# Kernel tuning notes

Measured on AMD Instinct MI355X. Metric: run time of the kernel, lower is better.

The kernel has to match this reference:

```python
import jax, jax.numpy as jnp
import numpy as np

E = 250000          # num_edges
T = 1500000         # num_triplets
H = 128             # hidden_dim
NB = 8              # num_bilinear
NS = 7              # num_spherical
NR = 6              # num_radial
OUT = 128           # output_dim


def silu(x):
    return x * jax.nn.sigmoid(x)


def setup_inputs() -> dict:
    key = jax.random.key(0)
    ks = jax.random.split(key, 24)
    s = 1.0 / np.sqrt(H)
    inp = {
        "x": jax.random.normal(ks[0], (E, H), jnp.float32),
        "rbf": jax.random.uniform(ks[1], (E, NR), jnp.float32),
        "sbf": jax.random.uniform(ks[2], (T, NS * NR), jnp.float32),
        "idx_kj": jax.random.randint(ks[3], (T,), 0, E, jnp.int32),
        "idx_ji": jax.random.randint(ks[4], (T,), 0, E, jnp.int32),
        # weights stored [in, out] (math identical to torch y = x @ W.T + b)
        "lin_rbf_w": jax.random.normal(ks[5], (NR, H), jnp.float32) * (1.0 / np.sqrt(NR)),
        "lin_sbf_w": jax.random.normal(ks[6], (NS * NR, NB), jnp.float32) * (1.0 / np.sqrt(NS * NR)),
        "lin_kj_w": jax.random.normal(ks[7], (H, H), jnp.float32) * s,
        "lin_kj_b": jnp.zeros((H,), jnp.float32),
        "lin_ji_w": jax.random.normal(ks[8], (H, H), jnp.float32) * s,
        "lin_ji_b": jnp.zeros((H,), jnp.float32),
        "W": jax.random.normal(ks[9], (H, NB, H), jnp.float32) * (2.0 / H),
        "rb_w1": jax.random.normal(ks[10], (H, H), jnp.float32) * s,
        "rb_b1": jnp.zeros((H,), jnp.float32),
        "rb_w2": jax.random.normal(ks[11], (H, H), jnp.float32) * s,
        "rb_b2": jnp.zeros((H,), jnp.float32),
        "lin_w": jax.random.normal(ks[12], (H, H), jnp.float32) * s,
        "lin_b": jnp.zeros((H,), jnp.float32),
        "ra1_w1": jax.random.normal(ks[13], (H, H), jnp.float32) * s,
        "ra1_b1": jnp.zeros((H,), jnp.float32),
        "ra1_w2": jax.random.normal(ks[14], (H, H), jnp.float32) * s,
        "ra1_b2": jnp.zeros((H,), jnp.float32),
        "ra2_w1": jax.random.normal(ks[15], (H, H), jnp.float32) * s,
        "ra2_b1": jnp.zeros((H,), jnp.float32),
        "ra2_w2": jax.random.normal(ks[16], (H, H), jnp.float32) * s,
        "ra2_b2": jnp.zeros((H,), jnp.float32),
        "lin_out_w": jax.random.normal(ks[17], (H, OUT), jnp.float32) * s,
        "lin_out_b": jnp.zeros((OUT,), jnp.float32),
    }
    return inp


def _residual(h, w1, b1, w2, b2):
    return h + silu(silu(h @ w1 + b1) @ w2 + b2)


def reference(x, rbf, sbf, idx_kj, idx_ji,
              lin_rbf_w, lin_sbf_w, lin_kj_w, lin_kj_b, lin_ji_w, lin_ji_b, W,
              rb_w1, rb_b1, rb_w2, rb_b2, lin_w, lin_b,
              ra1_w1, ra1_b1, ra1_w2, ra1_b2, ra2_w1, ra2_b1, ra2_w2, ra2_b2,
              lin_out_w, lin_out_b):
    rbf_h = rbf @ lin_rbf_w                      # [E, H]
    sbf_h = sbf @ lin_sbf_w                      # [T, NB]
    x_ji = silu(x @ lin_ji_w + lin_ji_b)         # [E, H]
    x_kj = silu(x @ lin_kj_w + lin_kj_b) * rbf_h # [E, H]
    xk = x_kj[idx_kj]                            # gather -> [T, H]
    # trilinear einsum 'wj,wl,ijl->wi' without materializing [T, NB, H]:
    # loop over the small bilinear axis (NB=8), each step a [T,H]@[H,H] matmul
    out_t = jnp.zeros_like(xk)
    for j in range(NB):
        out_t = out_t + sbf_h[:, j:j + 1] * (xk @ W[:, j, :].T)   # [T, H]
    agg = jax.ops.segment_sum(out_t, idx_ji, num_segments=x.shape[0])  # [E, H]
    h = x_ji + agg
    h = _residual(h, rb_w1, rb_b1, rb_w2, rb_b2)
    h = silu(h @ lin_w + lin_b) + x
    h = _residual(h, ra1_w1, ra1_b1, ra1_w2, ra1_b2)
    h = _residual(h, ra2_w1, ra2_b1, ra2_w2, ra2_b2)
    return silu(h @ lin_out_w + lin_out_b)
```

## Files before the change

kernel.cpp:

```cpp
#include <hip/hip_runtime.h>

#define EDGES 250000
#define TRIP  1500000
#define HD    128
#define NBIL  8
#define NSR   42
#define NRAD  6

__device__ __forceinline__ float silu_f(float v) {
  return v / (1.0f + __expf(-v));
}

#define GET4(v,i) ((i)==0?(v).x:((i)==1?(v).y:((i)==2?(v).z:(v).w)))


__global__ void k_hist(const int* __restrict__ idxji, int* __restrict__ hist) {
  const int t = blockIdx.x * 256 + threadIdx.x;
  if (t < TRIP) atomicAdd(&hist[idxji[t]], 1);
}

__global__ __launch_bounds__(256) void k_scan1(const int* __restrict__ hist, int* __restrict__ blks) {
  __shared__ int sd[256];
  const int tid = threadIdx.x;
  const long base = (long)blockIdx.x * 1024 + tid * 4;
  int s = 0;
#pragma unroll
  for (int u = 0; u < 4; ++u) { const long i = base + u; if (i < EDGES) s += hist[i]; }
  sd[tid] = s; __syncthreads();
  for (int off = 128; off > 0; off >>= 1) { if (tid < off) sd[tid] += sd[tid + off]; __syncthreads(); }
  if (tid == 0) blks[blockIdx.x] = sd[0];
}

__global__ __launch_bounds__(256) void k_scan2(int* __restrict__ blks, int n) {
  __shared__ int sd[256];
  const int tid = threadIdx.x;
  const int v = (tid < n) ? blks[tid] : 0;
  sd[tid] = v; __syncthreads();
  for (int off = 1; off < 256; off <<= 1) {
    const int t = (tid >= off) ? sd[tid - off] : 0;
    __syncthreads();
    sd[tid] += t;
    __syncthreads();
  }
  if (tid < n) blks[tid] = sd[tid] - v;
}

__global__ __launch_bounds__(256) void k_scan3(int* __restrict__ cursor, const int* __restrict__ blks,
                                               int* __restrict__ offs) {
  __shared__ int sd[256];
  const int tid = threadIdx.x;
  const long base = (long)blockIdx.x * 1024 + tid * 4;
  int v[4]; int s = 0;
#pragma unroll
  for (int u = 0; u < 4; ++u) { const long i = base + u; v[u] = (i < EDGES) ? cursor[i] : 0; s += v[u]; }
  sd[tid] = s; __syncthreads();
  for (int off = 1; off < 256; off <<= 1) {
    const int tv = (tid >= off) ? sd[tid - off] : 0;
    __syncthreads();
    sd[tid] += tv;
    __syncthreads();
  }
  int run = blks[blockIdx.x] + sd[tid] - s;
#pragma unroll
  for (int u = 0; u < 4; ++u) {
    const long i = base + u;
    if (i < EDGES) { offs[i] = run; cursor[i] = run; }
    run += v[u];
  }
  if (blockIdx.x == 0 && tid == 0) offs[EDGES] = TRIP;
}

__global__ void k_scatter(const int* __restrict__ idxji, const int* __restrict__ idxkj,
                          int* __restrict__ cursor, int* __restrict__ gkj, int* __restrict__ tpos) {
  const int t = blockIdx.x * 256 + threadIdx.x;
  if (t < TRIP) {
    const int e = idxji[t];
    const int pos = atomicAdd(&cursor[e], 1);
    gkj[pos] = idxkj[t];
    tpos[t] = pos;
  }
}


__global__ void k_wt(const float* __restrict__ W, float* __restrict__ wt) {
  const int idx = blockIdx.x * 256 + threadIdx.x;
  if (idx < NBIL * HD * HD) {
    const int i = idx & (HD - 1);
    const int k = idx >> 7;
    const int j = k >> 7;
    const int l = k & (HD - 1);
    wt[idx] = W[((long)i * NBIL + j) * HD + l];
  }
}


__global__ __launch_bounds__(256) void k_sbfh(const float* __restrict__ sbf,
    const float* __restrict__ sw, const int* __restrict__ tpos, float* __restrict__ outp) {
  __shared__ float ss[256 * NSR];
  __shared__ float wls[NSR * NBIL];
  const int tid = threadIdx.x;
  const long t0 = (long)blockIdx.x * 256;
  const long gbase = t0 * NSR;
  for (int idx = tid; idx < 256 * NSR; idx += 256) {
    const long gi = gbase + idx;
    ss[idx] = (gi < (long)TRIP * NSR) ? sbf[gi] : 0.f;
  }
  for (int idx = tid; idx < NSR * NBIL; idx += 256) wls[idx] = sw[idx];
  __syncthreads();
  const long t = t0 + tid;
  if (t < TRIP) {
    float o[NBIL] = {};
    for (int r = 0; r < NSR; ++r) {
      const float sv = ss[tid * NSR + r];
#pragma unroll
      for (int j = 0; j < NBIL; ++j) o[j] += sv * wls[r * NBIL + j];
    }
    const long p = tpos[t];
    *(float4*)(outp + p * 8) = make_float4(o[0], o[1], o[2], o[3]);
    *(float4*)(outp + p * 8 + 4) = make_float4(o[4], o[5], o[6], o[7]);
  }
}


__global__ __launch_bounds__(256, 4) void k_edge(const float* __restrict__ x,
    const float* __restrict__ rbf, const float* __restrict__ rbfw,
    const float* __restrict__ wji, const float* __restrict__ bji,
    const float* __restrict__ wkj, const float* __restrict__ bkj,
    float* __restrict__ xji, float* __restrict__ xkj) {
  __shared__ float xs[32][HD + 4];
  __shared__ float rbfs[32][NRAD];
  __shared__ float rws[NRAD][HD];
  const int tid = threadIdx.x;
  const long e0 = (long)blockIdx.x * 32;
  for (int idx = tid; idx < 32 * (HD / 4); idx += 256) {
    const int el = idx >> 5; const int k4 = (idx & 31) << 2;
    const long e = e0 + el;
    float4 v = make_float4(0.f, 0.f, 0.f, 0.f);
    if (e < EDGES) v = *(const float4*)(x + e * HD + k4);
    *(float4*)&xs[el][k4] = v;
  }
  for (int idx = tid; idx < 32 * NRAD; idx += 256) {
    const int el = idx / NRAD, r = idx % NRAD;
    const long e = e0 + el;
    rbfs[el][r] = (e < EDGES) ? rbf[e * NRAD + r] : 0.f;
  }
  for (int idx = tid; idx < NRAD * HD; idx += 256) rws[idx / HD][idx % HD] = rbfw[idx];
  __syncthreads();
  const int cg = tid & 15, eg = tid >> 4;
  const int i0 = cg * 8;
  float aj[2][8] = {}, ak[2][8] = {};
  for (int k = 0; k < HD; k += 4) {
    const float4 xv0 = *(const float4*)&xs[eg * 2 + 0][k];
    const float4 xv1 = *(const float4*)&xs[eg * 2 + 1][k];
#pragma unroll
    for (int dk = 0; dk < 4; ++dk) {
      const float4 j0 = *(const float4*)(wji + (long)(k + dk) * HD + i0);
      const float4 j1 = *(const float4*)(wji + (long)(k + dk) * HD + i0 + 4);
      const float4 q0 = *(const float4*)(wkj + (long)(k + dk) * HD + i0);
      const float4 q1 = *(const float4*)(wkj + (long)(k + dk) * HD + i0 + 4);
      const float a0 = GET4(xv0, dk), a1 = GET4(xv1, dk);
#pragma unroll
      for (int c = 0; c < 4; ++c) {
        const float wja = GET4(j0, c), wjb = GET4(j1, c);
        const float wka = GET4(q0, c), wkb = GET4(q1, c);
        aj[0][c] += a0 * wja; aj[0][c + 4] += a0 * wjb;
        aj[1][c] += a1 * wja; aj[1][c + 4] += a1 * wjb;
        ak[0][c] += a0 * wka; ak[0][c + 4] += a0 * wkb;
        ak[1][c] += a1 * wka; ak[1][c + 4] += a1 * wkb;
      }
    }
  }
  const float4 bj0 = *(const float4*)(bji + i0), bj1 = *(const float4*)(bji + i0 + 4);
  const float4 bk0 = *(const float4*)(bkj + i0), bk1 = *(const float4*)(bkj + i0 + 4);
#pragma unroll
  for (int a = 0; a < 2; ++a) {
    const int el = eg * 2 + a;
    const long e = e0 + el;
    if (e >= EDGES) continue;
    float rh[8];
#pragma unroll
    for (int c = 0; c < 8; ++c) rh[c] = 0.f;
#pragma unroll
    for (int r = 0; r < NRAD; ++r) {
      const float rv = rbfs[el][r];
#pragma unroll
      for (int c = 0; c < 8; ++c) rh[c] += rv * rws[r][i0 + c];
    }
    float oj[8], ok[8];
#pragma unroll
    for (int c = 0; c < 4; ++c) {
      oj[c]     = silu_f(aj[a][c]     + GET4(bj0, c));
      oj[c + 4] = silu_f(aj[a][c + 4] + GET4(bj1, c));
      ok[c]     = silu_f(ak[a][c]     + GET4(bk0, c)) * rh[c];
      ok[c + 4] = silu_f(ak[a][c + 4] + GET4(bk1, c)) * rh[c + 4];
    }
    *(float4*)(xji + e * HD + i0)     = make_float4(oj[0], oj[1], oj[2], oj[3]);
    *(float4*)(xji + e * HD + i0 + 4) = make_float4(oj[4], oj[5], oj[6], oj[7]);
    *(float4*)(xkj + e * HD + i0)     = make_float4(ok[0], ok[1], ok[2], ok[3]);
    *(float4*)(xkj + e * HD + i0 + 4) = make_float4(ok[4], ok[5], ok[6], ok[7]);
  }
}


#define FMA16(sA, sB, xv) do { \
  m[0]  += (sA).x * (xv).x;  m[1]  += (sA).x * (xv).y; \
  m[2]  += (sA).y * (xv).x;  m[3]  += (sA).y * (xv).y; \
  m[4]  += (sA).z * (xv).x;  m[5]  += (sA).z * (xv).y; \
  m[6]  += (sA).w * (xv).x;  m[7]  += (sA).w * (xv).y; \
  m[8]  += (sB).x * (xv).x;  m[9]  += (sB).x * (xv).y; \
  m[10] += (sB).y * (xv).x;  m[11] += (sB).y * (xv).y; \
  m[12] += (sB).z * (xv).x;  m[13] += (sB).z * (xv).y; \
  m[14] += (sB).w * (xv).x;  m[15] += (sB).w * (xv).y; } while (0)

#define ACCUM_SEGMENT(t0, t1) \
    int t = (t0); \
    for (; t + 4 <= (t1); t += 4) { \
      const int g0 = gkj[t], g1 = gkj[t + 1], g2 = gkj[t + 2], g3 = gkj[t + 3]; \
      const float2 x0 = *(const float2*)(xkj + (long)g0 * HD + l2); \
      const float2 x1 = *(const float2*)(xkj + (long)g1 * HD + l2); \
      const float2 x2 = *(const float2*)(xkj + (long)g2 * HD + l2); \
      const float2 x3 = *(const float2*)(xkj + (long)g3 * HD + l2); \
      const float4 sa0 = *(const float4*)(sbfp + (long)t * 8); \
      const float4 sb0 = *(const float4*)(sbfp + (long)t * 8 + 4); \
      const float4 sa1 = *(const float4*)(sbfp + (long)(t + 1) * 8); \
      const float4 sb1 = *(const float4*)(sbfp + (long)(t + 1) * 8 + 4); \
      const float4 sa2 = *(const float4*)(sbfp + (long)(t + 2) * 8); \
      const float4 sb2 = *(const float4*)(sbfp + (long)(t + 2) * 8 + 4); \
      const float4 sa3 = *(const float4*)(sbfp + (long)(t + 3) * 8); \
      const float4 sb3 = *(const float4*)(sbfp + (long)(t + 3) * 8 + 4); \
      FMA16(sa0, sb0, x0); \
      FMA16(sa1, sb1, x1); \
      FMA16(sa2, sb2, x2); \
      FMA16(sa3, sb3, x3); \
    } \
    for (; t < (t1); ++t) { \
      const int g = gkj[t]; \
      const float2 xv = *(const float2*)(xkj + (long)g * HD + l2); \
      const float4 sa = *(const float4*)(sbfp + (long)t * 8); \
      const float4 sb = *(const float4*)(sbfp + (long)t * 8 + 4); \
      FMA16(sa, sb, xv); \
    }

__global__ __launch_bounds__(256, 4) void k_mA(const float* __restrict__ xkj,
    const float* __restrict__ sbfp, const int* __restrict__ gkj,
    const int* __restrict__ offs, float* __restrict__ M, int e0chunk, int ecount) {
  const int tid = threadIdx.x;
  const int lane = tid & 63;
  const int wv = tid >> 6;
  const int er = blockIdx.x * 4 + wv;
  if (er >= ecount) return;
  const long e = (long)e0chunk + er;
  const int l2 = lane * 2;
  float m[16];
#pragma unroll
  for (int q = 0; q < 16; ++q) m[q] = 0.f;
  const int t0 = offs[e], t1 = offs[e + 1];
  { ACCUM_SEGMENT(t0, t1) }
#pragma unroll
  for (int j = 0; j < 8; ++j)
    *(float2*)(M + (long)er * 1024 + j * 128 + l2) = make_float2(m[2 * j], m[2 * j + 1]);
}

#define KC 32

__global__ __launch_bounds__(256, 4) void k_mB(const float* __restrict__ M,
    const float* __restrict__ wt, const float* __restrict__ xji,
    float* __restrict__ hout, int e0chunk, int ecount) {
  __shared__ float ms[128][KC + 4];
  __shared__ float ws[KC][HD + 4];
  const int tid = threadIdx.x;
  const int rbase = blockIdx.x * 128;
  const int cg = tid & 15, eg = tid >> 4;
  const int i0 = cg * 8;
  const int mc4 = (tid & 7) << 2;
  const int mrow = tid >> 3;
  const int wc4 = (tid & 31) << 2;
  const int wkr = tid >> 5;
  float acc[8][8] = {};
  for (int kc = 0; kc < 1024; kc += KC) {
    __syncthreads();
#pragma unroll
    for (int rr = 0; rr < 4; ++rr) {
      const int r = mrow + rr * 32;
      const int grow = rbase + r;
      float4 v = make_float4(0.f, 0.f, 0.f, 0.f);
      if (grow < ecount) v = *(const float4*)(M + (long)grow * 1024 + kc + mc4);
      *(float4*)&ms[r][mc4] = v;
    }
#pragma unroll
    for (int kk = 0; kk < 4; ++kk) {
      const int k = wkr * 4 + kk;
      *(float4*)&ws[k][wc4] = *(const float4*)(wt + (long)(kc + k) * HD + wc4);
    }
    __syncthreads();
    for (int k4 = 0; k4 < KC; k4 += 4) {
      float4 w[8];
#pragma unroll
      for (int dk = 0; dk < 4; ++dk) {
        w[2 * dk]     = *(const float4*)&ws[k4 + dk][i0];
        w[2 * dk + 1] = *(const float4*)&ws[k4 + dk][i0 + 4];
      }
#pragma unroll
      for (int ri = 0; ri < 8; ++ri) {
        const float4 mv = *(const float4*)&ms[eg + 16 * ri][k4];
#pragma unroll
        for (int dk = 0; dk < 4; ++dk) {
          const float a = GET4(mv, dk);
          const float4 wa = w[2 * dk], wb = w[2 * dk + 1];
          acc[ri][0] += a * wa.x; acc[ri][1] += a * wa.y;
          acc[ri][2] += a * wa.z; acc[ri][3] += a * wa.w;
          acc[ri][4] += a * wb.x; acc[ri][5] += a * wb.y;
          acc[ri][6] += a * wb.z; acc[ri][7] += a * wb.w;
        }
      }
    }
  }
#pragma unroll
  for (int ri = 0; ri < 8; ++ri) {
    const int row = rbase + eg + 16 * ri;
    if (row >= ecount) continue;
    const long e = (long)e0chunk + row;
    const float4 xa = *(const float4*)(xji + e * HD + i0);
    const float4 xb = *(const float4*)(xji + e * HD + i0 + 4);
    *(float4*)(hout + e * HD + i0)     = make_float4(acc[ri][0] + xa.x, acc[ri][1] + xa.y,
                                                     acc[ri][2] + xa.z, acc[ri][3] + xa.w);
    *(float4*)(hout + e * HD + i0 + 4) = make_float4(acc[ri][4] + xb.x, acc[ri][5] + xb.y,
                                                     acc[ri][6] + xb.z, acc[ri][7] + xb.w);
  }
}


__global__ __launch_bounds__(256, 2) void k_m(const float* __restrict__ xkj,
    const float* __restrict__ sbfp, const int* __restrict__ gkj,
    const int* __restrict__ offs, const float* __restrict__ wt,
    const float* __restrict__ xji, float* __restrict__ hout) {
  __shared__ float Mt[16][1024];
  const int tid = threadIdx.x;
  const int lane = tid & 63;
  const int wv = tid >> 6;
  const long e0 = (long)blockIdx.x * 16;
  const int l2 = lane * 2;
#pragma unroll 1
  for (int es = 0; es < 4; ++es) {
    const int el = wv * 4 + es;
    const long e = e0 + el;
    float m[16];
#pragma unroll
    for (int q = 0; q < 16; ++q) m[q] = 0.f;
    const int t0 = offs[e], t1 = offs[e + 1];
    { ACCUM_SEGMENT(t0, t1) }
#pragma unroll
    for (int j = 0; j < 8; ++j)
      *(float2*)&Mt[el][j * 128 + l2] = make_float2(m[2 * j], m[2 * j + 1]);
  }
  __syncthreads();
  const int cg = tid & 15, er = tid >> 4;
  const int i0 = cg * 8;
  float acc[8] = {};
  for (int kk = 0; kk < 1024; kk += 4) {
    const float4 mv = *(const float4*)&Mt[er][kk];
#pragma unroll
    for (int dk = 0; dk < 4; ++dk) {
      const float4 w0 = *(const float4*)(wt + (long)(kk + dk) * HD + i0);
      const float4 w1 = *(const float4*)(wt + (long)(kk + dk) * HD + i0 + 4);
      const float md = GET4(mv, dk);
      acc[0] += md * w0.x; acc[1] += md * w0.y; acc[2] += md * w0.z; acc[3] += md * w0.w;
      acc[4] += md * w1.x; acc[5] += md * w1.y; acc[6] += md * w1.z; acc[7] += md * w1.w;
    }
  }
  const long e = e0 + er;
  const float4 xa = *(const float4*)(xji + e * HD + i0);
  const float4 xb = *(const float4*)(xji + e * HD + i0 + 4);
  *(float4*)(hout + e * HD + i0)     = make_float4(acc[0] + xa.x, acc[1] + xa.y, acc[2] + xa.z, acc[3] + xa.w);
  *(float4*)(hout + e * HD + i0 + 4) = make_float4(acc[4] + xb.x, acc[5] + xb.y, acc[6] + xb.z, acc[7] + xb.w);
}


template<bool ADD>
__global__ __launch_bounds__(256, 4) void k_gemm(const float* __restrict__ in,
    const float* __restrict__ w, const float* __restrict__ bias,
    const float* __restrict__ addsrc, float* __restrict__ out) {
  __shared__ float xs[64][HD + 4];
  const int tid = threadIdx.x;
  const long e0 = (long)blockIdx.x * 64;
  for (int idx = tid; idx < 64 * (HD / 4); idx += 256) {
    const int el = idx >> 5; const int k4 = (idx & 31) << 2;
    const long e = e0 + el;
    float4 v = make_float4(0.f, 0.f, 0.f, 0.f);
    if (e < EDGES) v = *(const float4*)(in + e * HD + k4);
    *(float4*)&xs[el][k4] = v;
  }
  __syncthreads();
  const int cg = tid & 15, eg = tid >> 4;
  const int i0 = cg * 8;
  float acc[4][8] = {};
  for (int k = 0; k < HD; k += 4) {
    const float4 xv0 = *(const float4*)&xs[eg * 4 + 0][k];
    const float4 xv1 = *(const float4*)&xs[eg * 4 + 1][k];
    const float4 xv2 = *(const float4*)&xs[eg * 4 + 2][k];
    const float4 xv3 = *(const float4*)&xs[eg * 4 + 3][k];
#pragma unroll
    for (int dk = 0; dk < 4; ++dk) {
      const float4 w0 = *(const float4*)(w + (long)(k + dk) * HD + i0);
      const float4 w1 = *(const float4*)(w + (long)(k + dk) * HD + i0 + 4);
      const float a0 = GET4(xv0, dk), a1 = GET4(xv1, dk), a2 = GET4(xv2, dk), a3 = GET4(xv3, dk);
#pragma unroll
      for (int c = 0; c < 4; ++c) {
        const float wa = GET4(w0, c), wb = GET4(w1, c);
        acc[0][c] += a0 * wa; acc[0][c + 4] += a0 * wb;
        acc[1][c] += a1 * wa; acc[1][c + 4] += a1 * wb;
        acc[2][c] += a2 * wa; acc[2][c + 4] += a2 * wb;
        acc[3][c] += a3 * wa; acc[3][c + 4] += a3 * wb;
      }
    }
  }
  const float4 b0 = *(const float4*)(bias + i0);
  const float4 b1 = *(const float4*)(bias + i0 + 4);
#pragma unroll
  for (int a = 0; a < 4; ++a) {
    const long e = e0 + eg * 4 + a;
    if (e >= EDGES) continue;
    float o[8];
#pragma unroll
    for (int c = 0; c < 4; ++c) {
      o[c]     = silu_f(acc[a][c]     + GET4(b0, c));
      o[c + 4] = silu_f(acc[a][c + 4] + GET4(b1, c));
    }
    if (ADD) {
      const float4 ad0 = *(const float4*)(addsrc + e * HD + i0);
      const float4 ad1 = *(const float4*)(addsrc + e * HD + i0 + 4);
#pragma unroll
      for (int c = 0; c < 4; ++c) { o[c] += GET4(ad0, c); o[c + 4] += GET4(ad1, c); }
    }
    *(float4*)(out + e * HD + i0)     = make_float4(o[0], o[1], o[2], o[3]);
    *(float4*)(out + e * HD + i0 + 4) = make_float4(o[4], o[5], o[6], o[7]);
  }
}


__global__ __launch_bounds__(256, 2) void k_res(const float* __restrict__ in,
    const float* __restrict__ w1, const float* __restrict__ b1,
    const float* __restrict__ w2, const float* __restrict__ b2,
    float* __restrict__ out) {
  __shared__ float xs[64][HD + 4];
  __shared__ float ts[64][HD + 4];
  const int tid = threadIdx.x;
  const long e0 = (long)blockIdx.x * 64;
  for (int idx = tid; idx < 64 * (HD / 4); idx += 256) {
    const int el = idx >> 5; const int k4 = (idx & 31) << 2;
    const long e = e0 + el;
    float4 v = make_float4(0.f, 0.f, 0.f, 0.f);
    if (e < EDGES) v = *(const float4*)(in + e * HD + k4);
    *(float4*)&xs[el][k4] = v;
  }
  __syncthreads();
  const int cg = tid & 15, eg = tid >> 4;
  const int i0 = cg * 8;
  {
    float acc[4][8] = {};
    for (int k = 0; k < HD; k += 4) {
      const float4 xv0 = *(const float4*)&xs[eg * 4 + 0][k];
      const float4 xv1 = *(const float4*)&xs[eg * 4 + 1][k];
      const float4 xv2 = *(const float4*)&xs[eg * 4 + 2][k];
      const float4 xv3 = *(const float4*)&xs[eg * 4 + 3][k];
#pragma unroll
      for (int dk = 0; dk < 4; ++dk) {
        const float4 w0 = *(const float4*)(w1 + (long)(k + dk) * HD + i0);
        const float4 w1v = *(const float4*)(w1 + (long)(k + dk) * HD + i0 + 4);
        const float a0 = GET4(xv0, dk), a1 = GET4(xv1, dk), a2 = GET4(xv2, dk), a3 = GET4(xv3, dk);
#pragma unroll
        for (int c = 0; c < 4; ++c) {
          const float wa = GET4(w0, c), wb = GET4(w1v, c);
          acc[0][c] += a0 * wa; acc[0][c + 4] += a0 * wb;
          acc[1][c] += a1 * wa; acc[1][c + 4] += a1 * wb;
          acc[2][c] += a2 * wa; acc[2][c + 4] += a2 * wb;
          acc[3][c] += a3 * wa; acc[3][c + 4] += a3 * wb;
        }
      }
    }
    const float4 c0 = *(const float4*)(b1 + i0);
    const float4 c1 = *(const float4*)(b1 + i0 + 4);
#pragma unroll
    for (int a = 0; a < 4; ++a) {
      float o[8];
#pragma unroll
      for (int c = 0; c < 4; ++c) {
        o[c]     = silu_f(acc[a][c]     + GET4(c0, c));
        o[c + 4] = silu_f(acc[a][c + 4] + GET4(c1, c));
      }
      *(float4*)&ts[eg * 4 + a][i0]     = make_float4(o[0], o[1], o[2], o[3]);
      *(float4*)&ts[eg * 4 + a][i0 + 4] = make_float4(o[4], o[5], o[6], o[7]);
    }
  }
  __syncthreads();
  {
    float acc[4][8] = {};
    for (int k = 0; k < HD; k += 4) {
      const float4 xv0 = *(const float4*)&ts[eg * 4 + 0][k];
      const float4 xv1 = *(const float4*)&ts[eg * 4 + 1][k];
      const float4 xv2 = *(const float4*)&ts[eg * 4 + 2][k];
      const float4 xv3 = *(const float4*)&ts[eg * 4 + 3][k];
#pragma unroll
      for (int dk = 0; dk < 4; ++dk) {
        const float4 w0 = *(const float4*)(w2 + (long)(k + dk) * HD + i0);
        const float4 w1v = *(const float4*)(w2 + (long)(k + dk) * HD + i0 + 4);
        const float a0 = GET4(xv0, dk), a1 = GET4(xv1, dk), a2 = GET4(xv2, dk), a3 = GET4(xv3, dk);
#pragma unroll
        for (int c = 0; c < 4; ++c) {
          const float wa = GET4(w0, c), wb = GET4(w1v, c);
          acc[0][c] += a0 * wa; acc[0][c + 4] += a0 * wb;
          acc[1][c] += a1 * wa; acc[1][c + 4] += a1 * wb;
          acc[2][c] += a2 * wa; acc[2][c + 4] += a2 * wb;
          acc[3][c] += a3 * wa; acc[3][c + 4] += a3 * wb;
        }
      }
    }
    const float4 c0 = *(const float4*)(b2 + i0);
    const float4 c1 = *(const float4*)(b2 + i0 + 4);
#pragma unroll
    for (int a = 0; a < 4; ++a) {
      const long e = e0 + eg * 4 + a;
      if (e >= EDGES) continue;
      float o[8];
#pragma unroll
      for (int c = 0; c < 4; ++c) {
        o[c]     = silu_f(acc[a][c]     + GET4(c0, c)) + xs[eg * 4 + a][i0 + c];
        o[c + 4] = silu_f(acc[a][c + 4] + GET4(c1, c)) + xs[eg * 4 + a][i0 + 4 + c];
      }
      *(float4*)(out + e * HD + i0)     = make_float4(o[0], o[1], o[2], o[3]);
      *(float4*)(out + e * HD + i0 + 4) = make_float4(o[4], o[5], o[6], o[7]);
    }
  }
}


extern "C" void kernel_launch(void* const* d_in, const int* in_sizes, int n_in,
                              void* d_out, int out_size, void* d_ws, size_t ws_size,
                              hipStream_t stream) {
  const float* x         = (const float*)d_in[0];
  const float* rbf       = (const float*)d_in[1];
  const float* sbf       = (const float*)d_in[2];
  const int*   idx_kj    = (const int*)d_in[3];
  const int*   idx_ji    = (const int*)d_in[4];
  const float* lin_rbf_w = (const float*)d_in[5];
  const float* lin_sbf_w = (const float*)d_in[6];
  const float* lin_kj_w  = (const float*)d_in[7];
  const float* lin_kj_b  = (const float*)d_in[8];
  const float* lin_ji_w  = (const float*)d_in[9];
  const float* lin_ji_b  = (const float*)d_in[10];
  const float* Wtri      = (const float*)d_in[11];
  const float* rb_w1 = (const float*)d_in[12];
  const float* rb_b1 = (const float*)d_in[13];
  const float* rb_w2 = (const float*)d_in[14];
  const float* rb_b2 = (const float*)d_in[15];
  const float* lin_w = (const float*)d_in[16];
  const float* lin_b = (const float*)d_in[17];
  const float* ra1_w1 = (const float*)d_in[18];
  const float* ra1_b1 = (const float*)d_in[19];
  const float* ra1_w2 = (const float*)d_in[20];
  const float* ra1_b2 = (const float*)d_in[21];
  const float* ra2_w1 = (const float*)d_in[22];
  const float* ra2_b1 = (const float*)d_in[23];
  const float* ra2_w2 = (const float*)d_in[24];
  const float* ra2_b2 = (const float*)d_in[25];
  const float* lin_out_w = (const float*)d_in[26];
  const float* lin_out_b = (const float*)d_in[27];
  float* outp = (float*)d_out;

  const size_t EH = (size_t)EDGES * HD;
  float* buf0 = (float*)d_ws;
  float* buf1 = buf0 + EH;
  float* buf2 = buf1 + EH;
  float* sbfp = buf2 + EH;
  float* wt   = sbfp + (size_t)TRIP * NBIL;
  float* fend = wt + (size_t)NBIL * HD * HD;
  int* offs   = (int*)fend;
  int* cursor = offs + (EDGES + 4);
  int* gkj    = cursor + EDGES;
  int* tpos   = gkj + TRIP;
  int* blks   = tpos + TRIP;
  int* iend   = blks + 256;
  const size_t base_bytes = (size_t)((char*)iend - (char*)d_ws);
  const size_t moff = (base_bytes + 255) & ~(size_t)255;
  float* Mbuf = (float*)((char*)d_ws + moff);
  long ce = 0;
  if ((long)ws_size > (long)moff) {
    ce = ((long)ws_size - (long)moff) / (1024 * 4);
    ce &= ~127L;
    if (ce > 250112) ce = 250112;
  }
  const bool split = (ce >= 8192);

  hipMemsetAsync(cursor, 0, EDGES * sizeof(int), stream);
  const int TB  = (TRIP + 255) / 256;
  const int SCB = (EDGES + 1023) / 1024;
  k_hist<<<TB, 256, 0, stream>>>(idx_ji, cursor);
  k_scan1<<<SCB, 256, 0, stream>>>(cursor, blks);
  k_scan2<<<1, 256, 0, stream>>>(blks, SCB);
  k_scan3<<<SCB, 256, 0, stream>>>(cursor, blks, offs);
  k_scatter<<<TB, 256, 0, stream>>>(idx_ji, idx_kj, cursor, gkj, tpos);
  k_wt<<<(NBIL * HD * HD + 255) / 256, 256, 0, stream>>>(Wtri, wt);
  k_sbfh<<<TB, 256, 0, stream>>>(sbf, lin_sbf_w, tpos, sbfp);
  k_edge<<<(EDGES + 31) / 32, 256, 0, stream>>>(x, rbf, lin_rbf_w,
      lin_ji_w, lin_ji_b, lin_kj_w, lin_kj_b, buf0, buf1);

  if (split) {
    for (long c0 = 0; c0 < EDGES; c0 += ce) {
      const int ecount = (int)((EDGES - c0 < ce) ? (EDGES - c0) : ce);
      k_mA<<<(ecount + 3) / 4, 256, 0, stream>>>(buf1, sbfp, gkj, offs, Mbuf, (int)c0, ecount);
      k_mB<<<(ecount + 127) / 128, 256, 0, stream>>>(Mbuf, wt, buf0, buf2, (int)c0, ecount);
    }
  } else {
    k_m<<<EDGES / 16, 256, 0, stream>>>(buf1, sbfp, gkj, offs, wt, buf0, buf2);
  }

  const int GB = (EDGES + 63) / 64;
  k_res<<<GB, 256, 0, stream>>>(buf2, rb_w1, rb_b1, rb_w2, rb_b2, buf0);
  k_gemm<true ><<<GB, 256, 0, stream>>>(buf0, lin_w, lin_b, x, buf1);
  k_res<<<GB, 256, 0, stream>>>(buf1, ra1_w1, ra1_b1, ra1_w2, ra1_b2, buf2);
  k_res<<<GB, 256, 0, stream>>>(buf2, ra2_w1, ra2_b1, ra2_w2, ra2_b2, buf0);
  k_gemm<false><<<GB, 256, 0, stream>>>(buf0, lin_out_w, lin_out_b, nullptr, outp);
}
```

Measured before the change: 3.978 ms.

## Prefetch next K-chunk into registers and split column mapping in k_mB GEMM

The k_mB tiled GEMM now loads the next 32-wide K chunk of M and the weights into registers while the current chunk is being computed, then writes them to LDS at the top of the next iteration. This hides global-load latency behind the FMA loop. Each thread's 8 output columns are split into two groups of 4 at c0 and c0+64 instead of 8 contiguous, which changes the LDS access pattern to reduce bank conflicts. Occupancy hint is lowered from 4 to 3 blocks per CU to leave room for the extra prefetch registers.

```diff
diff --git a/kernel.cpp b/kernel.cpp
--- a/kernel.cpp
+++ b/kernel.cpp
@@ -263,7 +263,7 @@
 
 #define KC 32
 
-__global__ __launch_bounds__(256, 4) void k_mB(const float* __restrict__ M,
+__global__ __launch_bounds__(256, 3) void k_mB(const float* __restrict__ M,
     const float* __restrict__ wt, const float* __restrict__ xji,
     float* __restrict__ hout, int e0chunk, int ecount) {
   __shared__ float ms[128][KC + 4];
@@ -271,34 +271,49 @@
   const int tid = threadIdx.x;
   const int rbase = blockIdx.x * 128;
   const int cg = tid & 15, eg = tid >> 4;
-  const int i0 = cg * 8;
+  const int c0 = cg * 4;
   const int mc4 = (tid & 7) << 2;
   const int mrow = tid >> 3;
   const int wc4 = (tid & 31) << 2;
   const int wkr = tid >> 5;
+  float4 mreg[4], wreg[4];
+#pragma unroll
+  for (int rr = 0; rr < 4; ++rr) {
+    const int grow = rbase + mrow + rr * 32;
+    mreg[rr] = (grow < ecount) ? *(const float4*)(M + (long)grow * 1024 + mc4)
+                               : make_float4(0.f, 0.f, 0.f, 0.f);
+  }
+#pragma unroll
+  for (int kk = 0; kk < 4; ++kk)
+    wreg[kk] = *(const float4*)(wt + (long)(wkr * 4 + kk) * HD + wc4);
+
   float acc[8][8] = {};
   for (int kc = 0; kc < 1024; kc += KC) {
+#pragma unroll
+    for (int rr = 0; rr < 4; ++rr)
+      *(float4*)&ms[mrow + rr * 32][mc4] = mreg[rr];
+#pragma unroll
+    for (int kk = 0; kk < 4; ++kk)
+      *(float4*)&ws[wkr * 4 + kk][wc4] = wreg[kk];
     __syncthreads();
-#pragma unroll
-    for (int rr = 0; rr < 4; ++rr) {
-      const int r = mrow + rr * 32;
-      const int grow = rbase + r;
-      float4 v = make_float4(0.f, 0.f, 0.f, 0.f);
-      if (grow < ecount) v = *(const float4*)(M + (long)grow * 1024 + kc + mc4);
-      *(float4*)&ms[r][mc4] = v;
-    }
-#pragma unroll
-    for (int kk = 0; kk < 4; ++kk) {
-      const int k = wkr * 4 + kk;
-      *(float4*)&ws[k][wc4] = *(const float4*)(wt + (long)(kc + k) * HD + wc4);
-    }
-    __syncthreads();
+    const int kn = kc + KC;
+    if (kn < 1024) {
+#pragma unroll
+      for (int rr = 0; rr < 4; ++rr) {
+        const int grow = rbase + mrow + rr * 32;
+        mreg[rr] = (grow < ecount) ? *(const float4*)(M + (long)grow * 1024 + kn + mc4)
+                                   : make_float4(0.f, 0.f, 0.f, 0.f);
+      }
+#pragma unroll
+      for (int kk = 0; kk < 4; ++kk)
+        wreg[kk] = *(const float4*)(wt + (long)(kn + wkr * 4 + kk) * HD + wc4);
+    }
     for (int k4 = 0; k4 < KC; k4 += 4) {
-      float4 w[8];
+      float4 wlo[4], whi[4];
 #pragma unroll
       for (int dk = 0; dk < 4; ++dk) {
-        w[2 * dk]     = *(const float4*)&ws[k4 + dk][i0];
-        w[2 * dk + 1] = *(const float4*)&ws[k4 + dk][i0 + 4];
+        wlo[dk] = *(const float4*)&ws[k4 + dk][c0];
+        whi[dk] = *(const float4*)&ws[k4 + dk][c0 + 64];
       }
 #pragma unroll
       for (int ri = 0; ri < 8; ++ri) {
@@ -306,7 +321,7 @@
 #pragma unroll
         for (int dk = 0; dk < 4; ++dk) {
           const float a = GET4(mv, dk);
-          const float4 wa = w[2 * dk], wb = w[2 * dk + 1];
+          const float4 wa = wlo[dk], wb = whi[dk];
           acc[ri][0] += a * wa.x; acc[ri][1] += a * wa.y;
           acc[ri][2] += a * wa.z; acc[ri][3] += a * wa.w;
           acc[ri][4] += a * wb.x; acc[ri][5] += a * wb.y;
@@ -314,18 +329,19 @@
         }
       }
     }
+    __syncthreads();
   }
 #pragma unroll
   for (int ri = 0; ri < 8; ++ri) {
     const int row = rbase + eg + 16 * ri;
     if (row >= ecount) continue;
     const long e = (long)e0chunk + row;
-    const float4 xa = *(const float4*)(xji + e * HD + i0);
-    const float4 xb = *(const float4*)(xji + e * HD + i0 + 4);
-    *(float4*)(hout + e * HD + i0)     = make_float4(acc[ri][0] + xa.x, acc[ri][1] + xa.y,
-                                                     acc[ri][2] + xa.z, acc[ri][3] + xa.w);
-    *(float4*)(hout + e * HD + i0 + 4) = make_float4(acc[ri][4] + xb.x, acc[ri][5] + xb.y,
-                                                     acc[ri][6] + xb.z, acc[ri][7] + xb.w);
+    const float4 xa = *(const float4*)(xji + e * HD + c0);
+    const float4 xb = *(const float4*)(xji + e * HD + c0 + 64);
+    *(float4*)(hout + e * HD + c0)      = make_float4(acc[ri][0] + xa.x, acc[ri][1] + xa.y,
+                                                      acc[ri][2] + xa.z, acc[ri][3] + xa.w);
+    *(float4*)(hout + e * HD + c0 + 64) = make_float4(acc[ri][4] + xb.x, acc[ri][5] + xb.y,
+                                                      acc[ri][6] + xb.z, acc[ri][7] + xb.w);
   }
 }
 
```

Measured after the change: 4.037 ms. No clear change (+1.5%).
